# Kernel tuning notes

Measured on AMD Instinct MI355X. Metric: run time of the kernel, lower is better.

Reference implementation:

```python
import jax, jax.numpy as jnp
import numpy as np

B, T, C = 2, 2048, 2048
H, KVH, HD = 16, 4, 128  # heads, kv heads, head_dim
G = H // KVH             # GQA group size
THETA = 10000.0


def _rope_cos_sin(t, hd, dtype):
    inv_freq = 1.0 / (THETA ** (jnp.arange(0, hd, 2, dtype=jnp.float32) / hd))
    pos = jnp.arange(t, dtype=jnp.float32)
    freqs = pos[:, None] * inv_freq[None, :]          # [T, hd/2]
    emb = jnp.concatenate([freqs, freqs], axis=-1)    # [T, hd]
    return jnp.cos(emb).astype(dtype), jnp.sin(emb).astype(dtype)


def _rotate_half(x):
    x1, x2 = jnp.split(x, 2, axis=-1)
    return jnp.concatenate([-x2, x1], axis=-1)


def setup_inputs() -> dict:
    key = jax.random.key(0)
    ks = jax.random.split(key, 5)
    s_in = 1.0 / np.sqrt(C)
    return {
        "x": jax.random.normal(ks[0], (B, T, C), jnp.float32),
        "wq": jax.random.normal(ks[1], (C, H * HD), jnp.float32) * s_in,
        "bq": jnp.zeros((H * HD,), jnp.float32),
        "wk": jax.random.normal(ks[2], (C, KVH * HD), jnp.float32) * s_in,
        "bk": jnp.zeros((KVH * HD,), jnp.float32),
        "wv": jax.random.normal(ks[3], (C, KVH * HD), jnp.float32) * s_in,
        "bv": jnp.zeros((KVH * HD,), jnp.float32),
        "wo": jax.random.normal(ks[4], (H * HD, C), jnp.float32) * (1.0 / np.sqrt(H * HD)),
    }


def reference(x, wq, bq, wk, bk, wv, bv, wo):
    b, t, c = x.shape
    q = (x @ wq + bq).reshape(b, t, H, HD).transpose(0, 2, 1, 3)    # [B,H,T,hd]
    k = (x @ wk + bk).reshape(b, t, KVH, HD).transpose(0, 2, 1, 3)  # [B,KVH,T,hd]
    v = (x @ wv + bv).reshape(b, t, KVH, HD).transpose(0, 2, 1, 3)

    cos, sin = _rope_cos_sin(t, HD, x.dtype)  # [T,hd]
    q = q * cos + _rotate_half(q) * sin
    k = k * cos + _rotate_half(k) * sin

    # GQA: group query heads over kv heads
    qg = q.reshape(b, KVH, G, t, HD)
    scale = 1.0 / np.sqrt(HD)
    scores = jnp.einsum('bkgtd,bksd->bkgts', qg, k) * scale  # [B,KVH,G,T,T]
    causal = jnp.tril(jnp.ones((t, t), bool))
    scores = jnp.where(causal, scores, jnp.finfo(scores.dtype).min)
    attn = jax.nn.softmax(scores, axis=-1)
    out = jnp.einsum('bkgts,bksd->bkgtd', attn, v)            # [B,KVH,G,T,hd]
    out = out.reshape(b, H, t, HD).transpose(0, 2, 1, 3).reshape(b, t, H * HD)
    return out @ wo
```

## Files before the change

### kernel.cpp

```cpp
#include <hip/hip_runtime.h>
#include <hip/hip_bf16.h>
#include <math.h>

#define B_ 2
#define T_ 2048
#define C_ 2048
#define H_ 16
#define KVH_ 4
#define HD_ 128
#define G_ (H_ / KVH_)
#define MROWS (B_ * T_)
#define NQKV (H_ * HD_ + 2 * KVH_ * HD_)
#define KOFF (H_ * HD_)
#define VOFF (H_ * HD_ + KVH_ * HD_)

typedef __hip_bfloat16 bf16;
typedef short bf16x8 __attribute__((ext_vector_type(8)));
typedef short bf16x4 __attribute__((ext_vector_type(4)));
typedef float f32x4 __attribute__((ext_vector_type(4)));

__device__ __forceinline__ void gload_lds16(const void* g, void* l) {
  __builtin_amdgcn_global_load_lds(
      (const __attribute__((address_space(1))) unsigned int*)g,
      (__attribute__((address_space(3))) unsigned int*)l, 16, 0, 0);
}

static __device__ __forceinline__ f32x4 mfma32k(bf16x8 a, bf16x8 b, f32x4 c) {
  return __builtin_amdgcn_mfma_f32_16x16x32_bf16(a, b, c, 0, 0, 0);
}

static __device__ __forceinline__ f32x4 mfma16(bf16x4 a, bf16x4 b, f32x4 c) {
#if __has_builtin(__builtin_amdgcn_mfma_f32_16x16x16_bf16)
  return __builtin_amdgcn_mfma_f32_16x16x16_bf16(a, b, c, 0, 0, 0);
#else
  return __builtin_amdgcn_mfma_f32_16x16x16bf16_1k(a, b, c, 0, 0, 0);
#endif
}

static __device__ __forceinline__ short f2bf(float x) {
  unsigned u = __builtin_bit_cast(unsigned, x);
  u += 0x7FFFu + ((u >> 16) & 1u);
  return (short)(u >> 16);
}

static __device__ __forceinline__ float fexp2(float x) {
#if __has_builtin(__builtin_amdgcn_exp2f)
  return __builtin_amdgcn_exp2f(x);
#else
  return exp2f(x);
#endif
}

__global__ void cast_bf16_kernel(const float* __restrict__ in, bf16* __restrict__ out, int n) {
  int i = (blockIdx.x * 256 + threadIdx.x) * 4;
  if (i >= n) return;
  float4 v = *(const float4*)(in + i);
  out[i + 0] = __float2bfloat16(v.x);
  out[i + 1] = __float2bfloat16(v.y);
  out[i + 2] = __float2bfloat16(v.z);
  out[i + 3] = __float2bfloat16(v.w);
}

__global__ __launch_bounds__(256) void transpose_cast(const float* __restrict__ in,
                                                      bf16* __restrict__ out,
                                                      int R, int Ccols) {
  __shared__ float t[32][33];
  const int tx = threadIdx.x & 31, ty = threadIdx.x >> 5;
  const int r0 = blockIdx.y * 32, c0 = blockIdx.x * 32;
#pragma unroll
  for (int it = 0; it < 4; ++it)
    t[ty + 8 * it][tx] = in[(size_t)(r0 + ty + 8 * it) * Ccols + c0 + tx];
  __syncthreads();
#pragma unroll
  for (int it = 0; it < 4; ++it)
    out[(size_t)(c0 + ty + 8 * it) * R + r0 + tx] = __float2bfloat16(t[tx][ty + 8 * it]);
}

__global__ __launch_bounds__(256) void transpose_cast_qkvw(
    const float* __restrict__ wq, const float* __restrict__ wk,
    const float* __restrict__ wv, bf16* __restrict__ outT) {
  __shared__ float t[32][33];
  const int tx = threadIdx.x & 31, ty = threadIdx.x >> 5;
  const int r0 = blockIdx.y * 32;
  const int c0 = blockIdx.x * 32;
  const float* src;
  int nn, ld;
  if (c0 < KOFF)      { src = wq; nn = c0;        ld = 2048; }
  else if (c0 < VOFF) { src = wk; nn = c0 - KOFF; ld = 512; }
  else                { src = wv; nn = c0 - VOFF; ld = 512; }
#pragma unroll
  for (int it = 0; it < 4; ++it)
    t[ty + 8 * it][tx] = src[(size_t)(r0 + ty + 8 * it) * ld + nn + tx];
  __syncthreads();
#pragma unroll
  for (int it = 0; it < 4; ++it)
    outT[(size_t)(c0 + ty + 8 * it) * 2048 + r0 + tx] = __float2bfloat16(t[tx][ty + 8 * it]);
}

__global__ void rope_bf16(bf16* __restrict__ buf) {
  const int row = blockIdx.x / 20;
  const int hh = blockIdx.x % 20;
  const int t = row % T_;
  const int d = threadIdx.x;
  bf16* rp = buf + (size_t)row * NQKV + hh * HD_;
  float vd = __bfloat162float(rp[d]);
  float vp = __bfloat162float(rp[d ^ 64]);
  __syncthreads();
  const int i = d & 63;
  float invf = fexp2(-(float)i * (13.287712379549449f / 64.0f));
  float ang = (float)t * invf;
  float s, c;
  __sincosf(ang, &s, &c);
  rp[d] = __float2bfloat16((d < 64) ? (vd * c - vp * s) : (vd * c + vp * s));
}

__global__ __launch_bounds__(256) void pack_k(const bf16* __restrict__ qkv,
                                              bf16* __restrict__ kp) {
  const int tile = blockIdx.x & 63;
  const int bk = blockIdx.x >> 6;
  const int b = bk >> 2, kvh = bk & 3;
#pragma unroll
  for (int u = 0; u < 2; ++u) {
    const int t = threadIdx.x + u * 256;
    const int kc = t >> 6, L = t & 63;
    const bf16* src = qkv +
        (size_t)(b * T_ + tile * 32 + 16 * (kc >> 2) + (L & 15)) * NQKV +
        KOFF + kvh * HD_ + (kc & 3) * 32 + (L >> 4) * 8;
    bf16x8 v = *(const bf16x8*)src;
    *(bf16x8*)(kp + ((size_t)(bk * 64 + tile) * 8 + kc) * 512 + L * 8) = v;
  }
}

__global__ __launch_bounds__(256) void pack_v(const bf16* __restrict__ qkv,
                                              bf16* __restrict__ vp) {
  const int tile = blockIdx.x & 63;
  const int bk = blockIdx.x >> 6;
  const int b = bk >> 2, kvh = bk & 3;
#pragma unroll
  for (int u = 0; u < 2; ++u) {
    const int t = threadIdx.x + u * 256;
    const int ht = t >> 6, L = t & 63;
    const int colL = L & 15, quad = L >> 4;
    const bf16* base = qkv + (size_t)(b * T_ + tile * 32 + quad * 4) * NQKV +
                       VOFF + kvh * HD_ + ht * 16 + colL;
    bf16x8 v;
#pragma unroll
    for (int j = 0; j < 4; ++j) {
      v[j]     = *(const short*)(base + (size_t)j * NQKV);
      v[j + 4] = *(const short*)(base + (size_t)(16 + j) * NQKV);
    }
    *(bf16x8*)(vp + ((size_t)(bk * 64 + tile) * 8 + ht) * 512 + L * 8) = v;
  }
}

template <bool BF16OUT>
__global__ __launch_bounds__(256, 2) void gemm_mfma(
    const bf16* __restrict__ A, const bf16* __restrict__ Bt, void* __restrict__ Cout,
    const float* __restrict__ bq, const float* __restrict__ bk2,
    const float* __restrict__ bv2, int M, int N, int K) {
  __shared__ __align__(16) bf16 As[128 * 32];
  __shared__ __align__(16) bf16 Bs[128 * 32];
  const int tid = threadIdx.x;
  const int w = tid >> 6, lane = tid & 63;
  const int colL = lane & 15, quad = lane >> 4;
  const int wm = w & 1, wn = w >> 1;
  const int r0 = blockIdx.y * 128, c0 = blockIdx.x * 128;

  f32x4 acc[4][4];
  const f32x4 zero = {0.f, 0.f, 0.f, 0.f};
#pragma unroll
  for (int mt = 0; mt < 4; ++mt)
#pragma unroll
    for (int nt = 0; nt < 4; ++nt) acc[mt][nt] = zero;

  for (int k0 = 0; k0 < K; k0 += 32) {
    __syncthreads();
#pragma unroll
    for (int it = 0; it < 2; ++it) {
      const int seg = it * 4 + w;
      const int idx = seg * 64 + lane;
      const int row = idx >> 2, off = idx & 3;
      gload_lds16(A + (size_t)(r0 + row) * K + k0 + off * 8, &As[seg * 512]);
      gload_lds16(Bt + (size_t)(c0 + row) * K + k0 + off * 8, &Bs[seg * 512]);
    }
    __syncthreads();
    bf16x8 af[4], bfv[4];
#pragma unroll
    for (int mt = 0; mt < 4; ++mt)
      af[mt] = *(const bf16x8*)&As[(wm * 64 + mt * 16 + colL) * 32 + quad * 8];
#pragma unroll
    for (int nt = 0; nt < 4; ++nt)
      bfv[nt] = *(const bf16x8*)&Bs[(wn * 64 + nt * 16 + colL) * 32 + quad * 8];
#pragma unroll
    for (int mt = 0; mt < 4; ++mt)
#pragma unroll
      for (int nt = 0; nt < 4; ++nt)
        acc[mt][nt] =
            __builtin_amdgcn_mfma_f32_16x16x32_bf16(af[mt], bfv[nt], acc[mt][nt], 0, 0, 0);
  }

#pragma unroll
  for (int nt = 0; nt < 4; ++nt) {
    const int c = c0 + wn * 64 + nt * 16 + colL;
    float bias = 0.f;
    if (bq) bias = (c < KOFF) ? bq[c] : (c < VOFF ? bk2[c - KOFF] : bv2[c - VOFF]);
#pragma unroll
    for (int mt = 0; mt < 4; ++mt) {
#pragma unroll
      for (int i = 0; i < 4; ++i) {
        const int r = r0 + wm * 64 + mt * 16 + quad * 4 + i;
        const float v = acc[mt][nt][i] + bias;
        if (BF16OUT)
          ((bf16*)Cout)[(size_t)r * N + c] = __float2bfloat16(v);
        else
          ((float*)Cout)[(size_t)r * N + c] = v;
      }
    }
  }
}

#define FA_SCL2 (0.08838834764831845f * 1.4426950408889634f)
#define FA_M2 16.0f

__global__ __launch_bounds__(256, 3) void flash_mfma8(
    const bf16* __restrict__ qkv, const bf16* __restrict__ kp,
    const bf16* __restrict__ vp, bf16* __restrict__ ao) {
  __shared__ __align__(16) bf16 KS[3][4096];
  __shared__ __align__(16) bf16 VS[3][4096];

  const int id = blockIdx.x;
  const int bk = id & 7;
  const int u = id >> 3;
  const int jq = 127 - u;
  const int b = bk >> 2, kvh = bk & 3;
  const int w = threadIdx.x >> 6;
  const int h = (kvh << 2) | w;
  const int lane = threadIdx.x & 63;
  const int colL = lane & 15, quad = lane >> 4;
  const int myq0 = jq * 16;
  const int nkv = (jq >> 1) + 1;

  const bf16* kpt = kp + ((size_t)(bk * 64)) * 4096 + (w * 2) * 512 + lane * 8;
  const bf16* vpt = vp + ((size_t)(bk * 64)) * 4096 + (w * 2) * 512 + lane * 8;

  auto stageK = [&](int tile, int slot) {
    const bf16* s = kpt + (size_t)tile * 4096;
    bf16* d = &KS[slot][(w * 2) * 512];
    gload_lds16(s, d);
    gload_lds16(s + 512, d + 512);
  };
  auto stageV = [&](int tile, int slot) {
    const bf16* s = vpt + (size_t)tile * 4096;
    bf16* d = &VS[slot][(w * 2) * 512];
    gload_lds16(s, d);
    gload_lds16(s + 512, d + 512);
  };

  bf16x8 qf[4];
  {
    const bf16* qg = qkv + (size_t)(b * T_ + myq0) * NQKV + h * HD_;
#pragma unroll
    for (int c = 0; c < 4; ++c)
      qf[c] = *(const bf16x8*)(qg + (size_t)colL * NQKV + c * 32 + quad * 8);
  }

  const f32x4 zero = {0.f, 0.f, 0.f, 0.f};
  auto qk = [&](const bf16* Kb, f32x4 (&s_)[2]) {
    s_[0] = zero; s_[1] = zero;
#pragma unroll
    for (int c = 0; c < 4; ++c) {
      bf16x8 kf0 = *(const bf16x8*)(Kb + c * 512 + lane * 8);
      bf16x8 kf1 = *(const bf16x8*)(Kb + (4 + c) * 512 + lane * 8);
      s_[0] = mfma32k(kf0, qf[c], s_[0]);
      s_[1] = mfma32k(kf1, qf[c], s_[1]);
    }
  };

  f32x4 o[8];
#pragma unroll
  for (int ht = 0; ht < 8; ++ht) o[ht] = zero;
  float l_ = 0.f;

  stageK(0, 0);
  if (nkv > 1) stageK(1, 1);
  if (nkv > 2) stageK(2, 2);
  stageV(0, 0);
  if (nkv > 1) stageV(1, 1);
  asm volatile("s_waitcnt vmcnt(0)\n\ts_barrier" ::: "memory");

  f32x4 sA[2], sB[2];
  qk(KS[0], sA);

  int kStage = 0, kNext = 1, vRead = 0, vStage = 2;
#pragma unroll 1
  for (int tt = 0; tt < nkv; ++tt) {
    const bool sk = (tt + 3 < nkv), sv = (tt + 2 < nkv);
    if (sk) stageK(tt + 3, kStage);
    if (sv) stageV(tt + 2, vStage);

    if (tt + 1 < nkv) qk(KS[kNext], sB);

    bf16x4 pf[2];
    if (tt == nkv - 1) {
      const int qg = ((jq & 1) << 4) | colL;
#pragma unroll
      for (int kt = 0; kt < 2; ++kt) {
        const int kb = kt * 16 + quad * 4;
        float pv[4];
#pragma unroll
        for (int i = 0; i < 4; ++i) {
          float e = fexp2(fmaf(sA[kt][i], FA_SCL2, -FA_M2));
          pv[i] = (kb + i <= qg) ? e : 0.f;
        }
        l_ += (pv[0] + pv[1]) + (pv[2] + pv[3]);
        pf[kt] = (bf16x4){f2bf(pv[0]), f2bf(pv[1]), f2bf(pv[2]), f2bf(pv[3])};
      }
    } else {
#pragma unroll
      for (int kt = 0; kt < 2; ++kt) {
        float pv[4];
#pragma unroll
        for (int i = 0; i < 4; ++i)
          pv[i] = fexp2(fmaf(sA[kt][i], FA_SCL2, -FA_M2));
        l_ += (pv[0] + pv[1]) + (pv[2] + pv[3]);
        pf[kt] = (bf16x4){f2bf(pv[0]), f2bf(pv[1]), f2bf(pv[2]), f2bf(pv[3])};
      }
    }

    {
      const bf16* Vb = VS[vRead];
#pragma unroll
      for (int ht = 0; ht < 8; ++ht) {
        bf16x8 vf8 = *(const bf16x8*)(Vb + ht * 512 + lane * 8);
        bf16x4 lo = __builtin_shufflevector(vf8, vf8, 0, 1, 2, 3);
        bf16x4 hi = __builtin_shufflevector(vf8, vf8, 4, 5, 6, 7);
        o[ht] = mfma16(lo, pf[0], o[ht]);
        o[ht] = mfma16(hi, pf[1], o[ht]);
      }
    }

    if (sk)      asm volatile("s_waitcnt vmcnt(4)\n\ts_barrier" ::: "memory");
    else if (sv) asm volatile("s_waitcnt vmcnt(2)\n\ts_barrier" ::: "memory");
    else         asm volatile("s_waitcnt vmcnt(0)\n\ts_barrier" ::: "memory");

    sA[0] = sB[0]; sA[1] = sB[1];
    kStage = (kStage == 2) ? 0 : kStage + 1;
    kNext  = (kNext == 2) ? 0 : kNext + 1;
    vRead  = (vRead == 2) ? 0 : vRead + 1;
    vStage = (vStage == 2) ? 0 : vStage + 1;
  }

  {
    float lv = l_;
    lv += __shfl_xor(lv, 16);
    lv += __shfl_xor(lv, 32);
    const float rl = 1.f / lv;
    const size_t rbase = (size_t)(b * T_ + myq0 + colL) * (H_ * HD_) + h * HD_;
#pragma unroll
    for (int ht = 0; ht < 8; ++ht) {
      bf16x4 ov;
#pragma unroll
      for (int i = 0; i < 4; ++i) ov[i] = f2bf(o[ht][i] * rl);
      *(bf16x4*)(ao + rbase + ht * 16 + quad * 4) = ov;
    }
  }
}

extern "C" void kernel_launch(void* const* d_in, const int* in_sizes, int n_in,
                              void* d_out, int out_size, void* d_ws, size_t ws_size,
                              hipStream_t stream) {
  (void)in_sizes; (void)n_in; (void)out_size; (void)ws_size;
  const float* x  = (const float*)d_in[0];
  const float* wq = (const float*)d_in[1];
  const float* bq = (const float*)d_in[2];
  const float* wk = (const float*)d_in[3];
  const float* bk = (const float*)d_in[4];
  const float* wv = (const float*)d_in[5];
  const float* bv = (const float*)d_in[6];
  const float* wo = (const float*)d_in[7];
  float* out = (float*)d_out;

  char* ws = (char*)d_ws;
  bf16* xb    = (bf16*)ws;
  bf16* wqkvT = (bf16*)(ws + (16u << 20));
  bf16* woT   = (bf16*)(ws + (28u << 20));
  bf16* qkv   = (bf16*)(ws + (36u << 20));
  bf16* kp    = (bf16*)(ws + (60u << 20));
  bf16* vp    = (bf16*)(ws + (68u << 20));

  cast_bf16_kernel<<<dim3(MROWS * C_ / 1024), dim3(256), 0, stream>>>(x, xb, MROWS * C_);

  transpose_cast_qkvw<<<dim3(96, 64), dim3(256), 0, stream>>>(wq, wk, wv, wqkvT);
  transpose_cast<<<dim3(64, 64), dim3(256), 0, stream>>>(wo, woT, 2048, 2048);

  gemm_mfma<true><<<dim3(NQKV / 128, MROWS / 128), dim3(256), 0, stream>>>(
      xb, wqkvT, qkv, bq, bk, bv, MROWS, NQKV, C_);

  rope_bf16<<<dim3(MROWS * 20), dim3(128), 0, stream>>>(qkv);

  pack_k<<<dim3(8 * 64), dim3(256), 0, stream>>>(qkv, kp);
  pack_v<<<dim3(8 * 64), dim3(256), 0, stream>>>(qkv, vp);

  bf16* ao = xb;
  flash_mfma8<<<dim3(1024), dim3(256), 0, stream>>>(qkv, kp, vp, ao);

  gemm_mfma<false><<<dim3(C_ / 128, MROWS / 128), dim3(256), 0, stream>>>(
      ao, woT, out, nullptr, nullptr, nullptr, MROWS, C_, KOFF);
}
```

Measured before the change: 330.8 us.

## Fuse prep kernels and apply RoPE inside K packing and flash Q load

Merges the x cast, the two weight transpose-casts and a new cos/sin table build into a single prep launch. Removes the standalone RoPE pass over the whole QKV buffer: RoPE on K is now applied while packing K (pack_k and pack_v are fused into one launch), and RoPE on Q is applied when each flash block loads its Q fragments, using the precomputed table. This saves several kernel launches and a full read-modify-write of the QKV buffer. In exchange the flash kernel does extra table loads and arithmetic in its prologue.

```diff
diff --git a/kernel.cpp b/kernel.cpp
--- a/kernel.cpp
+++ b/kernel.cpp
@@ -13,6 +13,7 @@
 #define NQKV (H_ * HD_ + 2 * KVH_ * HD_)
 #define KOFF (H_ * HD_)
 #define VOFF (H_ * HD_ + KVH_ * HD_)
+#define L2T (13.287712379549449f / 64.0f)
 
 typedef __hip_bfloat16 bf16;
 typedef short bf16x8 __attribute__((ext_vector_type(8)));
@@ -43,6 +44,11 @@
   return (short)(u >> 16);
 }
 
+static __device__ __forceinline__ float bfh2f(short h) {
+  unsigned u = ((unsigned)(unsigned short)h) << 16;
+  return __builtin_bit_cast(float, u);
+}
+
 static __device__ __forceinline__ float fexp2(float x) {
 #if __has_builtin(__builtin_amdgcn_exp2f)
   return __builtin_amdgcn_exp2f(x);
@@ -51,105 +57,120 @@
 #endif
 }
 
-__global__ void cast_bf16_kernel(const float* __restrict__ in, bf16* __restrict__ out, int n) {
-  int i = (blockIdx.x * 256 + threadIdx.x) * 4;
-  if (i >= n) return;
-  float4 v = *(const float4*)(in + i);
-  out[i + 0] = __float2bfloat16(v.x);
-  out[i + 1] = __float2bfloat16(v.y);
-  out[i + 2] = __float2bfloat16(v.z);
-  out[i + 3] = __float2bfloat16(v.w);
-}
-
-__global__ __launch_bounds__(256) void transpose_cast(const float* __restrict__ in,
-                                                      bf16* __restrict__ out,
-                                                      int R, int Ccols) {
+__global__ __launch_bounds__(256) void prep_kernel(
+    const float* __restrict__ x, bf16* __restrict__ xb,
+    const float* __restrict__ wq, const float* __restrict__ wk,
+    const float* __restrict__ wv, bf16* __restrict__ wqkvT,
+    const float* __restrict__ wo, bf16* __restrict__ woT,
+    float2* __restrict__ tab) {
   __shared__ float t[32][33];
-  const int tx = threadIdx.x & 31, ty = threadIdx.x >> 5;
-  const int r0 = blockIdx.y * 32, c0 = blockIdx.x * 32;
-#pragma unroll
-  for (int it = 0; it < 4; ++it)
-    t[ty + 8 * it][tx] = in[(size_t)(r0 + ty + 8 * it) * Ccols + c0 + tx];
-  __syncthreads();
-#pragma unroll
-  for (int it = 0; it < 4; ++it)
-    out[(size_t)(c0 + ty + 8 * it) * R + r0 + tx] = __float2bfloat16(t[tx][ty + 8 * it]);
-}
-
-__global__ __launch_bounds__(256) void transpose_cast_qkvw(
-    const float* __restrict__ wq, const float* __restrict__ wk,
-    const float* __restrict__ wv, bf16* __restrict__ outT) {
-  __shared__ float t[32][33];
-  const int tx = threadIdx.x & 31, ty = threadIdx.x >> 5;
-  const int r0 = blockIdx.y * 32;
-  const int c0 = blockIdx.x * 32;
-  const float* src;
-  int nn, ld;
-  if (c0 < KOFF)      { src = wq; nn = c0;        ld = 2048; }
-  else if (c0 < VOFF) { src = wk; nn = c0 - KOFF; ld = 512; }
-  else                { src = wv; nn = c0 - VOFF; ld = 512; }
-#pragma unroll
-  for (int it = 0; it < 4; ++it)
-    t[ty + 8 * it][tx] = src[(size_t)(r0 + ty + 8 * it) * ld + nn + tx];
-  __syncthreads();
-#pragma unroll
-  for (int it = 0; it < 4; ++it)
-    outT[(size_t)(c0 + ty + 8 * it) * 2048 + r0 + tx] = __float2bfloat16(t[tx][ty + 8 * it]);
-}
-
-__global__ void rope_bf16(bf16* __restrict__ buf) {
-  const int row = blockIdx.x / 20;
-  const int hh = blockIdx.x % 20;
-  const int t = row % T_;
-  const int d = threadIdx.x;
-  bf16* rp = buf + (size_t)row * NQKV + hh * HD_;
-  float vd = __bfloat162float(rp[d]);
-  float vp = __bfloat162float(rp[d ^ 64]);
-  __syncthreads();
-  const int i = d & 63;
-  float invf = fexp2(-(float)i * (13.287712379549449f / 64.0f));
-  float ang = (float)t * invf;
-  float s, c;
-  __sincosf(ang, &s, &c);
-  rp[d] = __float2bfloat16((d < 64) ? (vd * c - vp * s) : (vd * c + vp * s));
-}
-
-__global__ __launch_bounds__(256) void pack_k(const bf16* __restrict__ qkv,
-                                              bf16* __restrict__ kp) {
-  const int tile = blockIdx.x & 63;
-  const int bk = blockIdx.x >> 6;
-  const int b = bk >> 2, kvh = bk & 3;
-#pragma unroll
-  for (int u = 0; u < 2; ++u) {
-    const int t = threadIdx.x + u * 256;
-    const int kc = t >> 6, L = t & 63;
-    const bf16* src = qkv +
-        (size_t)(b * T_ + tile * 32 + 16 * (kc >> 2) + (L & 15)) * NQKV +
-        KOFF + kvh * HD_ + (kc & 3) * 32 + (L >> 4) * 8;
-    bf16x8 v = *(const bf16x8*)src;
-    *(bf16x8*)(kp + ((size_t)(bk * 64 + tile) * 8 + kc) * 512 + L * 8) = v;
-  }
-}
-
-__global__ __launch_bounds__(256) void pack_v(const bf16* __restrict__ qkv,
-                                              bf16* __restrict__ vp) {
-  const int tile = blockIdx.x & 63;
-  const int bk = blockIdx.x >> 6;
-  const int b = bk >> 2, kvh = bk & 3;
-#pragma unroll
-  for (int u = 0; u < 2; ++u) {
-    const int t = threadIdx.x + u * 256;
-    const int ht = t >> 6, L = t & 63;
-    const int colL = L & 15, quad = L >> 4;
-    const bf16* base = qkv + (size_t)(b * T_ + tile * 32 + quad * 4) * NQKV +
-                       VOFF + kvh * HD_ + ht * 16 + colL;
-    bf16x8 v;
-#pragma unroll
-    for (int j = 0; j < 4; ++j) {
-      v[j]     = *(const short*)(base + (size_t)j * NQKV);
-      v[j + 4] = *(const short*)(base + (size_t)(16 + j) * NQKV);
-    }
-    *(bf16x8*)(vp + ((size_t)(bk * 64 + tile) * 8 + ht) * 512 + L * 8) = v;
+  int bid = blockIdx.x;
+  if (bid < 8192) {
+    const int i = (bid * 256 + threadIdx.x) * 4;
+    float4 v = *(const float4*)(x + i);
+    xb[i + 0] = __float2bfloat16(v.x);
+    xb[i + 1] = __float2bfloat16(v.y);
+    xb[i + 2] = __float2bfloat16(v.z);
+    xb[i + 3] = __float2bfloat16(v.w);
+    return;
+  }
+  bid -= 8192;
+  if (bid < 6144) {
+    const int tx = threadIdx.x & 31, ty = threadIdx.x >> 5;
+    const int c0 = (bid % 96) * 32;
+    const int r0 = (bid / 96) * 32;
+    const float* src;
+    int nn, ld;
+    if (c0 < KOFF)      { src = wq; nn = c0;        ld = 2048; }
+    else if (c0 < VOFF) { src = wk; nn = c0 - KOFF; ld = 512; }
+    else                { src = wv; nn = c0 - VOFF; ld = 512; }
+#pragma unroll
+    for (int it = 0; it < 4; ++it)
+      t[ty + 8 * it][tx] = src[(size_t)(r0 + ty + 8 * it) * ld + nn + tx];
+    __syncthreads();
+#pragma unroll
+    for (int it = 0; it < 4; ++it)
+      wqkvT[(size_t)(c0 + ty + 8 * it) * 2048 + r0 + tx] =
+          __float2bfloat16(t[tx][ty + 8 * it]);
+    return;
+  }
+  bid -= 6144;
+  if (bid < 4096) {
+    const int tx = threadIdx.x & 31, ty = threadIdx.x >> 5;
+    const int c0 = (bid & 63) * 32;
+    const int r0 = (bid >> 6) * 32;
+#pragma unroll
+    for (int it = 0; it < 4; ++it)
+      t[ty + 8 * it][tx] = wo[(size_t)(r0 + ty + 8 * it) * 2048 + c0 + tx];
+    __syncthreads();
+#pragma unroll
+    for (int it = 0; it < 4; ++it)
+      woT[(size_t)(c0 + ty + 8 * it) * 2048 + r0 + tx] =
+          __float2bfloat16(t[tx][ty + 8 * it]);
+    return;
+  }
+  bid -= 4096;
+  {
+    const int idx = bid * 256 + threadIdx.x;
+    const int tt = idx >> 6, i = idx & 63;
+    const float invf = fexp2(-(float)i * L2T);
+    float s, c;
+    __sincosf((float)tt * invf, &s, &c);
+    tab[idx] = make_float2(c, s);
+  }
+}
+
+__global__ __launch_bounds__(256) void pack_kv(const bf16* __restrict__ qkv,
+                                               bf16* __restrict__ kp,
+                                               bf16* __restrict__ vp,
+                                               const float2* __restrict__ tab) {
+  const int pid = blockIdx.x;
+  if (pid < 512) {
+    const int tile = pid & 63;
+    const int bk = pid >> 6;
+    const int b = bk >> 2, kvh = bk & 3;
+#pragma unroll
+    for (int u = 0; u < 2; ++u) {
+      const int t = threadIdx.x + u * 256;
+      const int kc = t >> 6, L = t & 63;
+      const int trow = tile * 32 + 16 * (kc >> 2) + (L & 15);
+      const bf16* src = qkv + (size_t)(b * T_ + trow) * NQKV +
+                        KOFF + kvh * HD_ + (kc & 3) * 32 + (L >> 4) * 8;
+      bf16x8 vs = *(const bf16x8*)src;
+      bf16x8 vpair = *(const bf16x8*)(src + (((kc & 2) == 0) ? 64 : -64));
+      const float2* tp = tab + trow * 64 + (kc & 1) * 32 + (L >> 4) * 8;
+      bf16x8 outv;
+#pragma unroll
+      for (int jj = 0; jj < 8; ++jj) {
+        const float2 cs = tp[jj];
+        const float a = bfh2f(vs[jj]), p = bfh2f(vpair[jj]);
+        outv[jj] = f2bf(((kc & 2) == 0) ? (a * cs.x - p * cs.y)
+                                        : (a * cs.x + p * cs.y));
+      }
+      *(bf16x8*)(kp + ((size_t)(bk * 64 + tile) * 8 + kc) * 512 + L * 8) = outv;
+    }
+    return;
+  }
+  {
+    const int pid2 = pid - 512;
+    const int tile = pid2 & 63;
+    const int bk = pid2 >> 6;
+    const int b = bk >> 2, kvh = bk & 3;
+#pragma unroll
+    for (int u = 0; u < 2; ++u) {
+      const int t = threadIdx.x + u * 256;
+      const int ht = t >> 6, L = t & 63;
+      const int colL = L & 15, quad = L >> 4;
+      const bf16* base = qkv + (size_t)(b * T_ + tile * 32 + quad * 4) * NQKV +
+                         VOFF + kvh * HD_ + ht * 16 + colL;
+      bf16x8 v;
+#pragma unroll
+      for (int jj = 0; jj < 4; ++jj) {
+        v[jj]     = *(const short*)(base + (size_t)jj * NQKV);
+        v[jj + 4] = *(const short*)(base + (size_t)(16 + jj) * NQKV);
+      }
+      *(bf16x8*)(vp + ((size_t)(bk * 64 + tile) * 8 + ht) * 512 + L * 8) = v;
+    }
   }
 }
 
@@ -224,7 +245,8 @@
 
 __global__ __launch_bounds__(256, 3) void flash_mfma8(
     const bf16* __restrict__ qkv, const bf16* __restrict__ kp,
-    const bf16* __restrict__ vp, bf16* __restrict__ ao) {
+    const bf16* __restrict__ vp, bf16* __restrict__ ao,
+    const float2* __restrict__ tab) {
   __shared__ __align__(16) bf16 KS[3][4096];
   __shared__ __align__(16) bf16 VS[3][4096];
 
@@ -259,9 +281,24 @@
   bf16x8 qf[4];
   {
     const bf16* qg = qkv + (size_t)(b * T_ + myq0) * NQKV + h * HD_;
+    bf16x8 rq[4];
 #pragma unroll
     for (int c = 0; c < 4; ++c)
-      qf[c] = *(const bf16x8*)(qg + (size_t)colL * NQKV + c * 32 + quad * 8);
+      rq[c] = *(const bf16x8*)(qg + (size_t)colL * NQKV + c * 32 + quad * 8);
+    const float2* tp = tab + (myq0 + colL) * 64 + quad * 8;
+    float2 cs0[8], cs1[8];
+#pragma unroll
+    for (int jj = 0; jj < 8; ++jj) { cs0[jj] = tp[jj]; cs1[jj] = tp[32 + jj]; }
+#pragma unroll
+    for (int c = 0; c < 4; ++c) {
+#pragma unroll
+      for (int jj = 0; jj < 8; ++jj) {
+        const float2 cs = (c & 1) ? cs1[jj] : cs0[jj];
+        const float a = bfh2f(rq[c][jj]), p = bfh2f(rq[c ^ 2][jj]);
+        qf[c][jj] = f2bf((c & 2) ? (a * cs.x + p * cs.y)
+                                 : (a * cs.x - p * cs.y));
+      }
+    }
   }
 
   const f32x4 zero = {0.f, 0.f, 0.f, 0.f};
@@ -387,22 +424,18 @@
   bf16* qkv   = (bf16*)(ws + (36u << 20));
   bf16* kp    = (bf16*)(ws + (60u << 20));
   bf16* vp    = (bf16*)(ws + (68u << 20));
-
-  cast_bf16_kernel<<<dim3(MROWS * C_ / 1024), dim3(256), 0, stream>>>(x, xb, MROWS * C_);
-
-  transpose_cast_qkvw<<<dim3(96, 64), dim3(256), 0, stream>>>(wq, wk, wv, wqkvT);
-  transpose_cast<<<dim3(64, 64), dim3(256), 0, stream>>>(wo, woT, 2048, 2048);
+  float2* tab = (float2*)(ws + (76u << 20));
+
+  prep_kernel<<<dim3(18944), dim3(256), 0, stream>>>(
+      x, xb, wq, wk, wv, wqkvT, wo, woT, tab);
 
   gemm_mfma<true><<<dim3(NQKV / 128, MROWS / 128), dim3(256), 0, stream>>>(
       xb, wqkvT, qkv, bq, bk, bv, MROWS, NQKV, C_);
 
-  rope_bf16<<<dim3(MROWS * 20), dim3(128), 0, stream>>>(qkv);
-
-  pack_k<<<dim3(8 * 64), dim3(256), 0, stream>>>(qkv, kp);
-  pack_v<<<dim3(8 * 64), dim3(256), 0, stream>>>(qkv, vp);
+  pack_kv<<<dim3(1024), dim3(256), 0, stream>>>(qkv, kp, vp, tab);
 
   bf16* ao = xb;
-  flash_mfma8<<<dim3(1024), dim3(256), 0, stream>>>(qkv, kp, vp, ao);
+  flash_mfma8<<<dim3(1024), dim3(256), 0, stream>>>(qkv, kp, vp, ao, tab);
 
   gemm_mfma<false><<<dim3(C_ / 128, MROWS / 128), dim3(256), 0, stream>>>(
       ao, woT, out, nullptr, nullptr, nullptr, MROWS, C_, KOFF);
```

Result: faster. 308.8 us (-6.7%).
